# Kernel tuning notes

Measured on AMD Instinct MI355X. Metric: run time of the kernel, lower is better.

Reference implementation:

```python
import jax, jax.numpy as jnp
import numpy as np

EPS = 1e-8  # matches torch.nn.functional.cosine_similarity default eps


def setup_inputs() -> dict:
    key = jax.random.key(0)
    k1, k2 = jax.random.split(key)
    B, C, L, D = 65536, 64, 64, 128
    x = jax.random.normal(k1, (B, D), dtype=jnp.float32)
    category_embeddings = jax.random.normal(k2, (C, L, D), dtype=jnp.float32)
    leaf_usage_counts = jnp.zeros((C, L), dtype=jnp.float32)
    return {
        "x": x,
        "category_embeddings": category_embeddings,
        "leaf_usage_counts": leaf_usage_counts,
    }


def reference(x, category_embeddings, leaf_usage_counts):
    # Cosine similarity: [B, C, L] without materializing the broadcast [B,C,L,D].
    x_norm = jnp.maximum(jnp.linalg.norm(x, axis=-1, keepdims=True), EPS)        # [B, 1]
    e_norm = jnp.maximum(jnp.linalg.norm(category_embeddings, axis=-1), EPS)     # [C, L]
    dots = jnp.einsum('bd,cld->bcl', x, category_embeddings)                     # [B, C, L]
    cosine_sim = dots / (x_norm[:, :, None] * e_norm[None, :, :])                # [B, C, L]

    # Training-path usage-count update (done under no_grad in torch):
    # per-category bincount of argmax leaf, scatter-added into the buffer.
    max_indices = jnp.argmax(cosine_sim, axis=2)                                 # [B, C] int
    C, L = leaf_usage_counts.shape
    cat_ids = jnp.broadcast_to(jnp.arange(C)[None, :], max_indices.shape)        # [B, C]
    leaf_counts = jnp.zeros((C, L), jnp.float32).at[cat_ids, max_indices].add(1.0)
    new_leaf_usage_counts = leaf_usage_counts + leaf_counts                      # [C, L]

    cosine_sim_max = jnp.max(cosine_sim, axis=2)                                 # [B, C]
    return cosine_sim_max, new_leaf_usage_counts
```

## Files before the change

kernel.cpp:

```cpp
#include <hip/hip_runtime.h>
#include <stdint.h>
#include <stddef.h>

#define D      128
#define NCATS  64
#define NLEAF  64
#define NC_BLK 4
#define BM     512
#define BIAS   32.0f

#define WS_E16_BYTES   (1u << 20)
#define WS_X16_BYTES   (16u << 20)
#define WS_XINV_BYTES  (65536u * 4u)
#define WS_NEEDED      ((size_t)WS_E16_BYTES + WS_X16_BYTES + WS_XINV_BYTES)

typedef _Float16 half8_t  __attribute__((ext_vector_type(8)));
typedef _Float16 half4h_t __attribute__((ext_vector_type(4)));
typedef float    float4_t __attribute__((ext_vector_type(4)));

__device__ __forceinline__ void async_ld16(const void* g, void* l) {
  __builtin_amdgcn_global_load_lds((const __attribute__((address_space(1))) uint32_t*)g,
                                   (__attribute__((address_space(3))) uint32_t*)l,
                                   16, 0, 0);
}

__device__ __forceinline__ unsigned umax2(unsigned a, unsigned b) { return a > b ? a : b; }
__device__ __forceinline__ unsigned umax3(unsigned a, unsigned b, unsigned c) {
  return umax2(umax2(a, b), c);
}

__global__ __launch_bounds__(256) void prep_kernel(const float* __restrict__ e,
                                                   const float* __restrict__ xf,
                                                   char* __restrict__ e16,
                                                   char* __restrict__ x16,
                                                   float* __restrict__ xinv,
                                                   const float* __restrict__ cin,
                                                   float* __restrict__ counts_out) {
  __shared__ __align__(16) half8_t xs[272];

  const int t  = threadIdx.x;
  const int rl = t >> 4;
  const int cc = t & 15;

  if (blockIdx.x < 256) {
    const int row = blockIdx.x * 16 + rl;
    const float* src = e + (size_t)row * D + cc * 8;
    float4_t v0 = *(const float4_t*)src;
    float4_t v1 = *(const float4_t*)(src + 4);
    float ss = v0.x*v0.x + v0.y*v0.y + v0.z*v0.z + v0.w*v0.w +
               v1.x*v1.x + v1.y*v1.y + v1.z*v1.z + v1.w*v1.w;
    ss += __shfl_xor(ss, 1);
    ss += __shfl_xor(ss, 2);
    ss += __shfl_xor(ss, 4);
    ss += __shfl_xor(ss, 8);
    const float inv = 1.0f / fmaxf(sqrtf(ss), 1e-8f);
    half8_t h;
    h[0] = (_Float16)(v0.x * inv); h[1] = (_Float16)(v0.y * inv);
    h[2] = (_Float16)(v0.z * inv); h[3] = (_Float16)(v0.w * inv);
    h[4] = (_Float16)(v1.x * inv); h[5] = (_Float16)(v1.y * inv);
    h[6] = (_Float16)(v1.z * inv); h[7] = (_Float16)(v1.w * inv);
    const int cat = row >> 6;
    const int rt  = (row >> 4) & 3;
    const int wl  = row & 15;
    const int s   = cc >> 2;
    const int q   = cc & 3;
    char* dst = e16 + (size_t)cat * 16384 + (rt * 4 + s) * 1024 + (q * 16 + wl) * 16;
    *(half8_t*)dst = h;
    if (blockIdx.x < (NCATS * NLEAF) / 256)
      counts_out[blockIdx.x * 256 + t] = cin[blockIdx.x * 256 + t];
  } else {
    const int g   = blockIdx.x - 256;
    const int row = g * 16 + rl;
    const float* src = xf + (size_t)row * D + cc * 8;
    float4_t v0 = *(const float4_t*)src;
    float4_t v1 = *(const float4_t*)(src + 4);
    float ss = v0.x*v0.x + v0.y*v0.y + v0.z*v0.z + v0.w*v0.w +
               v1.x*v1.x + v1.y*v1.y + v1.z*v1.z + v1.w*v1.w;
    ss += __shfl_xor(ss, 1);
    ss += __shfl_xor(ss, 2);
    ss += __shfl_xor(ss, 4);
    ss += __shfl_xor(ss, 8);
    const float inv = 1.0f / fmaxf(sqrtf(ss), 1e-8f);
    half8_t h;
    h[0] = (_Float16)v0.x; h[1] = (_Float16)v0.y;
    h[2] = (_Float16)v0.z; h[3] = (_Float16)v0.w;
    h[4] = (_Float16)v1.x; h[5] = (_Float16)v1.y;
    h[6] = (_Float16)v1.z; h[7] = (_Float16)v1.w;
    if (cc == 0) xinv[row] = inv;
    xs[t + (t >> 4)] = h;
    __syncthreads();
    const int tp = ((t & 15) << 4) | (t >> 4);
    half8_t hh = xs[tp + (tp >> 4)];
    *(half8_t*)(x16 + (size_t)g * 4096 + t * 16) = hh;
  }
}

template <bool XP>
__global__ __launch_bounds__(512, 4) void main_kernel(const float* __restrict__ x,
                                                      const char* __restrict__ e16,
                                                      const char* __restrict__ x16,
                                                      const float* __restrict__ xinv,
                                                      float* __restrict__ cos_out,
                                                      float* __restrict__ counts_out) {
  __shared__ __align__(16) char ebuf[2][16384];
  __shared__ unsigned hist[NC_BLK * NLEAF];
  __shared__ __align__(16) _Float16 stage[BM * NC_BLK];

  const int tid  = threadIdx.x;
  const int w    = tid >> 6;
  const int lane = tid & 63;
  const int q    = lane >> 4;
  const int wl   = lane & 15;

  const int xcd    = blockIdx.x & 7;
  const int rb     = xcd * 16 + ((blockIdx.x >> 3) & 15);
  const int c_base = (blockIdx.x >> 7) * NC_BLK;
  const int b_base = rb * BM;

  {
    const char* g = e16 + (size_t)(c_base + (w >> 2)) * 16384 + (w & 3) * 4096 + lane * 16;
    char* l = &ebuf[w >> 2][(w & 3) * 4096 + lane * 16];
#pragma unroll
    for (int j = 0; j < 4; ++j) async_ld16(g + j * 1024, l + j * 1024);
  }

  if (tid < NC_BLK * NLEAF) hist[tid] = 0;

  half8_t bfrag[4][4];
  float inv_x[4];
  if constexpr (XP) {
    const size_t gbase = ((size_t)b_base >> 4) + (size_t)w * 4;
#pragma unroll
    for (int nt = 0; nt < 4; ++nt) {
      const char* xr = x16 + (gbase + nt) * 4096 + q * 256 + wl * 16;
#pragma unroll
      for (int s = 0; s < 4; ++s)
        bfrag[nt][s] = *(const half8_t*)(xr + s * 1024);
      inv_x[nt] = xinv[b_base + w * 64 + nt * 16 + wl];
    }
  } else {
#pragma unroll
    for (int nt = 0; nt < 4; ++nt) {
      const int row = b_base + w * 64 + nt * 16 + wl;
      const float* xr = x + (size_t)row * D;
      float ss = 0.f;
#pragma unroll
      for (int s = 0; s < 4; ++s) {
        const float* p = xr + s * 32 + q * 8;
        float4_t v0 = *(const float4_t*)p;
        float4_t v1 = *(const float4_t*)(p + 4);
        half8_t h;
        h[0] = (_Float16)v0.x; h[1] = (_Float16)v0.y;
        h[2] = (_Float16)v0.z; h[3] = (_Float16)v0.w;
        h[4] = (_Float16)v1.x; h[5] = (_Float16)v1.y;
        h[6] = (_Float16)v1.z; h[7] = (_Float16)v1.w;
        bfrag[nt][s] = h;
        ss += v0.x*v0.x + v0.y*v0.y + v0.z*v0.z + v0.w*v0.w +
              v1.x*v1.x + v1.y*v1.y + v1.z*v1.z + v1.w*v1.w;
      }
      ss += __shfl_xor(ss, 16);
      ss += __shfl_xor(ss, 32);
      inv_x[nt] = 1.0f / fmaxf(sqrtf(ss), 1e-8f);
    }
  }

  const int lofs = lane * 16;
  const unsigned idq = (unsigned)(q << 2);
  const float4_t bias4 = {BIAS, BIAS, BIAS, BIAS};

  __syncthreads();

#pragma unroll
  for (int half = 0; half < 2; ++half) {
    if (half == 1) {
      __syncthreads();
      const char* g = e16 + (size_t)(c_base + 2 + (w >> 2)) * 16384 + (w & 3) * 4096 + lane * 16;
      char* l = &ebuf[w >> 2][(w & 3) * 4096 + lane * 16];
#pragma unroll
      for (int j = 0; j < 4; ++j) async_ld16(g + j * 1024, l + j * 1024);
      __syncthreads();
    }
#pragma unroll
    for (int sub = 0; sub < 2; ++sub) {
      const int ci = half * 2 + sub;
      const char* cur = &ebuf[sub][lofs];

      unsigned pk[4];
      __builtin_amdgcn_s_setprio(1);
#pragma unroll
      for (int rt = 0; rt < 4; ++rt) {
        float4_t acc[4];
#pragma unroll
        for (int s = 0; s < 4; ++s) {
          half8_t ef = *(const half8_t*)(cur + (rt * 4 + s) * 1024);
#pragma unroll
          for (int nt = 0; nt < 4; ++nt)
            acc[nt] = __builtin_amdgcn_mfma_f32_16x16x32_f16(
                ef, bfrag[nt][s], (s == 0) ? bias4 : acc[nt], 0, 0, 0);
        }
#pragma unroll
        for (int nt = 0; nt < 4; ++nt) {
          const unsigned k0 = (__float_as_uint(acc[nt][0]) & 0xFFFFFFC0u) | (unsigned)(rt * 16 + 0);
          const unsigned k1 = (__float_as_uint(acc[nt][1]) & 0xFFFFFFC0u) | (unsigned)(rt * 16 + 1);
          const unsigned k2 = (__float_as_uint(acc[nt][2]) & 0xFFFFFFC0u) | (unsigned)(rt * 16 + 2);
          const unsigned k3 = (__float_as_uint(acc[nt][3]) & 0xFFFFFFC0u) | (unsigned)(rt * 16 + 3);
          const unsigned m  = umax3(k0, k1, k2);
          pk[nt] = (rt == 0) ? umax2(m, k3) : umax3(m, k3, pk[nt]);
        }
      }
      __builtin_amdgcn_s_setprio(0);

#pragma unroll
      for (int nt = 0; nt < 4; ++nt) {
        unsigned v = pk[nt] | idq;
        unsigned t = (unsigned)__shfl_xor((int)v, 16);
        v = (v > t) ? v : t;
        t = (unsigned)__shfl_xor((int)v, 32);
        v = (v > t) ? v : t;
        pk[nt] = v;
      }

      {
        const unsigned pk01 = (q == 0) ? pk[0] : pk[1];
        const unsigned pk23 = (q == 2) ? pk[2] : pk[3];
        const unsigned pkq  = (q < 2) ? pk01 : pk23;
        const float    iv01 = (q == 0) ? inv_x[0] : inv_x[1];
        const float    iv23 = (q == 2) ? inv_x[2] : inv_x[3];
        const float    invq = (q < 2) ? iv01 : iv23;
        const float val = (__uint_as_float(pkq & 0xFFFFFFC0u) - BIAS) * invq;
        stage[tid * NC_BLK + ci] = (_Float16)val;
        atomicAdd(&hist[ci * NLEAF + (int)(pkq & 63u)], 1u);
      }
    }
  }

  __syncthreads();

  {
    half4h_t h = *(const half4h_t*)&stage[tid * NC_BLK];
    float4_t v;
    v.x = (float)h[0]; v.y = (float)h[1]; v.z = (float)h[2]; v.w = (float)h[3];
    *(float4_t*)&cos_out[(size_t)(b_base + tid) * NCATS + c_base] = v;
  }

  if (tid < NC_BLK * NLEAF) {
    const unsigned v = hist[tid];
    if (v) atomicAdd(&counts_out[c_base * NLEAF + tid], (float)v);
  }
}

extern "C" void kernel_launch(void* const* d_in, const int* in_sizes, int n_in,
                              void* d_out, int out_size, void* d_ws, size_t ws_size,
                              hipStream_t stream) {
  const float* x   = (const float*)d_in[0];
  const float* e   = (const float*)d_in[1];
  const float* cin = (const float*)d_in[2];

  const int B = in_sizes[0] / D;
  float* cos_out = (float*)d_out;
  float* counts_out = cos_out + (size_t)B * NCATS;

  char*  e16  = (char*)d_ws;
  char*  x16  = e16 + WS_E16_BYTES;
  float* xinv = (float*)(x16 + WS_X16_BYTES);

  const bool xp = (ws_size >= WS_NEEDED);
  const int prep_grid = xp ? (256 + B / 16) : 256;
  prep_kernel<<<prep_grid, 256, 0, stream>>>(e, x, e16, x16, xinv, cin, counts_out);

  const int main_grid = (B / BM) * (NCATS / NC_BLK);
  if (xp)
    main_kernel<true><<<main_grid, 512, 0, stream>>>(x, e16, x16, xinv, cos_out, counts_out);
  else
    main_kernel<false><<<main_grid, 512, 0, stream>>>(x, e16, x16, xinv, cos_out, counts_out);
}
```

Before: 142.0 us.

## Switch to 32x32x16 MFMA tiles with matching embedding layout

Replaces the 16x16x32 f16 MFMA tiling with 32x32x16 instructions. The prep kernel's fragment layout for embeddings changes to match, and the x fragment loads and argmax-key reduction are restructured to 16-element accumulators with fewer cross-lane shuffles. This is meant to cut the MFMA instruction count, fragment LDS reads and the shuffle reduction work. Launch bounds drop to 2 blocks per SM, since the larger accumulators raise register pressure, which may lower occupancy.

```diff
diff --git a/kernel.cpp b/kernel.cpp
--- a/kernel.cpp
+++ b/kernel.cpp
@@ -17,6 +17,7 @@
 typedef _Float16 half8_t  __attribute__((ext_vector_type(8)));
 typedef _Float16 half4h_t __attribute__((ext_vector_type(4)));
 typedef float    float4_t __attribute__((ext_vector_type(4)));
+typedef float    f32x16_t __attribute__((ext_vector_type(16)));
 
 __device__ __forceinline__ void async_ld16(const void* g, void* l) {
   __builtin_amdgcn_global_load_lds((const __attribute__((address_space(1))) uint32_t*)g,
@@ -60,11 +61,9 @@
     h[4] = (_Float16)(v1.x * inv); h[5] = (_Float16)(v1.y * inv);
     h[6] = (_Float16)(v1.z * inv); h[7] = (_Float16)(v1.w * inv);
     const int cat = row >> 6;
-    const int rt  = (row >> 4) & 3;
-    const int wl  = row & 15;
-    const int s   = cc >> 2;
-    const int q   = cc & 3;
-    char* dst = e16 + (size_t)cat * 16384 + (rt * 4 + s) * 1024 + (q * 16 + wl) * 16;
+    const int l   = ((cc & 1) << 5) | (row & 31);
+    const int f   = ((row >> 5) & 1) * 8 + (cc >> 1);
+    char* dst = e16 + (size_t)cat * 16384 + f * 1024 + l * 16;
     *(half8_t*)dst = h;
     if (blockIdx.x < (NCATS * NLEAF) / 256)
       counts_out[blockIdx.x * 256 + t] = cin[blockIdx.x * 256 + t];
@@ -96,7 +95,7 @@
 }
 
 template <bool XP>
-__global__ __launch_bounds__(512, 4) void main_kernel(const float* __restrict__ x,
+__global__ __launch_bounds__(512, 2) void main_kernel(const float* __restrict__ x,
                                                       const char* __restrict__ e16,
                                                       const char* __restrict__ x16,
                                                       const float* __restrict__ xinv,
@@ -109,8 +108,8 @@
   const int tid  = threadIdx.x;
   const int w    = tid >> 6;
   const int lane = tid & 63;
-  const int q    = lane >> 4;
-  const int wl   = lane & 15;
+  const int hi   = lane >> 5;
+  const int c32  = lane & 31;
 
   const int xcd    = blockIdx.x & 7;
   const int rb     = xcd * 16 + ((blockIdx.x >> 3) & 15);
@@ -126,27 +125,28 @@
 
   if (tid < NC_BLK * NLEAF) hist[tid] = 0;
 
-  half8_t bfrag[4][4];
-  float inv_x[4];
+  half8_t bfrag[2][8];
+  float inv_x[2];
   if constexpr (XP) {
-    const size_t gbase = ((size_t)b_base >> 4) + (size_t)w * 4;
-#pragma unroll
-    for (int nt = 0; nt < 4; ++nt) {
-      const char* xr = x16 + (gbase + nt) * 4096 + q * 256 + wl * 16;
-#pragma unroll
-      for (int s = 0; s < 4; ++s)
-        bfrag[nt][s] = *(const half8_t*)(xr + s * 1024);
-      inv_x[nt] = xinv[b_base + w * 64 + nt * 16 + wl];
+#pragma unroll
+    for (int nt = 0; nt < 2; ++nt) {
+      const int base32 = b_base + w * 64 + nt * 32;
+      const char* xr = x16 + (size_t)((base32 >> 4) + ((lane >> 4) & 1)) * 4096 +
+                       hi * 256 + (lane & 15) * 16;
+#pragma unroll
+      for (int s = 0; s < 8; ++s)
+        bfrag[nt][s] = *(const half8_t*)(xr + s * 512);
+      inv_x[nt] = xinv[base32 + c32];
     }
   } else {
 #pragma unroll
-    for (int nt = 0; nt < 4; ++nt) {
-      const int row = b_base + w * 64 + nt * 16 + wl;
-      const float* xr = x + (size_t)row * D;
+    for (int nt = 0; nt < 2; ++nt) {
+      const int base32 = b_base + w * 64 + nt * 32;
+      const float* xr = x + (size_t)(base32 + c32) * D;
       float ss = 0.f;
 #pragma unroll
-      for (int s = 0; s < 4; ++s) {
-        const float* p = xr + s * 32 + q * 8;
+      for (int s = 0; s < 8; ++s) {
+        const float* p = xr + s * 16 + hi * 8;
         float4_t v0 = *(const float4_t*)p;
         float4_t v1 = *(const float4_t*)(p + 4);
         half8_t h;
@@ -158,15 +158,15 @@
         ss += v0.x*v0.x + v0.y*v0.y + v0.z*v0.z + v0.w*v0.w +
               v1.x*v1.x + v1.y*v1.y + v1.z*v1.z + v1.w*v1.w;
       }
-      ss += __shfl_xor(ss, 16);
       ss += __shfl_xor(ss, 32);
       inv_x[nt] = 1.0f / fmaxf(sqrtf(ss), 1e-8f);
     }
   }
 
   const int lofs = lane * 16;
-  const unsigned idq = (unsigned)(q << 2);
-  const float4_t bias4 = {BIAS, BIAS, BIAS, BIAS};
+  const unsigned idq = (unsigned)(hi << 2);
+  const f32x16_t bias16 = {BIAS, BIAS, BIAS, BIAS, BIAS, BIAS, BIAS, BIAS,
+                           BIAS, BIAS, BIAS, BIAS, BIAS, BIAS, BIAS, BIAS};
 
   __syncthreads();
 
@@ -185,48 +185,59 @@
       const int ci = half * 2 + sub;
       const char* cur = &ebuf[sub][lofs];
 
-      unsigned pk[4];
+      unsigned pk0, pk1;
       __builtin_amdgcn_s_setprio(1);
 #pragma unroll
-      for (int rt = 0; rt < 4; ++rt) {
-        float4_t acc[4];
-#pragma unroll
-        for (int s = 0; s < 4; ++s) {
-          half8_t ef = *(const half8_t*)(cur + (rt * 4 + s) * 1024);
-#pragma unroll
-          for (int nt = 0; nt < 4; ++nt)
-            acc[nt] = __builtin_amdgcn_mfma_f32_16x16x32_f16(
-                ef, bfrag[nt][s], (s == 0) ? bias4 : acc[nt], 0, 0, 0);
+      for (int rt2 = 0; rt2 < 2; ++rt2) {
+        f32x16_t acc0, acc1;
+#pragma unroll
+        for (int s = 0; s < 8; ++s) {
+          half8_t ef = *(const half8_t*)(cur + (rt2 * 8 + s) * 1024);
+          acc0 = __builtin_amdgcn_mfma_f32_32x32x16_f16(ef, bfrag[0][s],
+                                                        (s == 0) ? bias16 : acc0, 0, 0, 0);
+          acc1 = __builtin_amdgcn_mfma_f32_32x32x16_f16(ef, bfrag[1][s],
+                                                        (s == 0) ? bias16 : acc1, 0, 0, 0);
         }
-#pragma unroll
-        for (int nt = 0; nt < 4; ++nt) {
-          const unsigned k0 = (__float_as_uint(acc[nt][0]) & 0xFFFFFFC0u) | (unsigned)(rt * 16 + 0);
-          const unsigned k1 = (__float_as_uint(acc[nt][1]) & 0xFFFFFFC0u) | (unsigned)(rt * 16 + 1);
-          const unsigned k2 = (__float_as_uint(acc[nt][2]) & 0xFFFFFFC0u) | (unsigned)(rt * 16 + 2);
-          const unsigned k3 = (__float_as_uint(acc[nt][3]) & 0xFFFFFFC0u) | (unsigned)(rt * 16 + 3);
-          const unsigned m  = umax3(k0, k1, k2);
-          pk[nt] = (rt == 0) ? umax2(m, k3) : umax3(m, k3, pk[nt]);
+#define KEY(A, R) ((__float_as_uint((A)[R]) & 0xFFFFFFC0u) | \
+                   (unsigned)(rt2 * 32 + ((R) & 3) + 8 * ((R) >> 2)))
+        {
+          unsigned m = umax3(KEY(acc0, 0), KEY(acc0, 1), KEY(acc0, 2));
+          m = umax3(m, KEY(acc0, 3), KEY(acc0, 4));
+          m = umax3(m, KEY(acc0, 5), KEY(acc0, 6));
+          m = umax3(m, KEY(acc0, 7), KEY(acc0, 8));
+          m = umax3(m, KEY(acc0, 9), KEY(acc0, 10));
+          m = umax3(m, KEY(acc0, 11), KEY(acc0, 12));
+          m = umax3(m, KEY(acc0, 13), KEY(acc0, 14));
+          m = umax2(m, KEY(acc0, 15));
+          pk0 = (rt2 == 0) ? m : umax2(pk0, m);
         }
+        {
+          unsigned m = umax3(KEY(acc1, 0), KEY(acc1, 1), KEY(acc1, 2));
+          m = umax3(m, KEY(acc1, 3), KEY(acc1, 4));
+          m = umax3(m, KEY(acc1, 5), KEY(acc1, 6));
+          m = umax3(m, KEY(acc1, 7), KEY(acc1, 8));
+          m = umax3(m, KEY(acc1, 9), KEY(acc1, 10));
+          m = umax3(m, KEY(acc1, 11), KEY(acc1, 12));
+          m = umax3(m, KEY(acc1, 13), KEY(acc1, 14));
+          m = umax2(m, KEY(acc1, 15));
+          pk1 = (rt2 == 0) ? m : umax2(pk1, m);
+        }
+#undef KEY
       }
       __builtin_amdgcn_s_setprio(0);
 
-#pragma unroll
-      for (int nt = 0; nt < 4; ++nt) {
-        unsigned v = pk[nt] | idq;
-        unsigned t = (unsigned)__shfl_xor((int)v, 16);
-        v = (v > t) ? v : t;
+      {
+        unsigned v = pk0 | idq;
+        unsigned t = (unsigned)__shfl_xor((int)v, 32);
+        pk0 = umax2(v, t);
+        v = pk1 | idq;
         t = (unsigned)__shfl_xor((int)v, 32);
-        v = (v > t) ? v : t;
-        pk[nt] = v;
+        pk1 = umax2(v, t);
       }
 
       {
-        const unsigned pk01 = (q == 0) ? pk[0] : pk[1];
-        const unsigned pk23 = (q == 2) ? pk[2] : pk[3];
-        const unsigned pkq  = (q < 2) ? pk01 : pk23;
-        const float    iv01 = (q == 0) ? inv_x[0] : inv_x[1];
-        const float    iv23 = (q == 2) ? inv_x[2] : inv_x[3];
-        const float    invq = (q < 2) ? iv01 : iv23;
+        const unsigned pkq = (hi == 0) ? pk0 : pk1;
+        const float    invq = (hi == 0) ? inv_x[0] : inv_x[1];
         const float val = (__uint_as_float(pkq & 0xFFFFFFC0u) - BIAS) * invq;
         stage[tid * NC_BLK + ci] = (_Float16)val;
         atomicAdd(&hist[ci * NLEAF + (int)(pkq & 63u)], 1u);
```

Result: slower. 151.9 us (+6.9%).
